# Kernel optimization log

Hardware: AMD Instinct MI355X
Metric: run time of the kernel (lower is better)

The kernel has to match this reference:

```python
import jax, jax.numpy as jnp
import numpy as np
from jax import lax

DIM = 8            # per-head dim
GROUPS = 192       # 3 * heads, groups of the pointwise aggreg conv
EPS_ATT = 1e-15
EPS_BN = 1e-5


def conv1x1(x, w):
    # x: (B,C,H,W), w: (O,C)
    return jnp.einsum('bchw,oc->bohw', x, w)


def setup_inputs() -> dict:
    key = jax.random.key(0)
    ks = jax.random.split(key, 9)
    B, C, H, W = 4, 512, 64, 64
    td3 = 3 * 512  # 3 * total_dim = 1536
    return {
        'x':       jax.random.normal(ks[0], (B, C, H, W), jnp.float32),
        'w_qkv':   jax.random.normal(ks[1], (td3, C), jnp.float32) * 0.05,
        'w_dw':    jax.random.normal(ks[2], (td3, 1, 5, 5), jnp.float32) * 0.05,
        'w_pw':    jax.random.normal(ks[3], (GROUPS, 8, 8), jnp.float32) * 0.05,
        'w_proj':  jax.random.normal(ks[4], (512, 1024), jnp.float32) * 0.05,
        'bn_gamma': 1.0 + 0.1 * jax.random.normal(ks[5], (512,), jnp.float32),
        'bn_beta': 0.1 * jax.random.normal(ks[6], (512,), jnp.float32),
        'bn_mean': 0.1 * jax.random.normal(ks[7], (512,), jnp.float32),
        'bn_var':  0.5 + jax.random.uniform(ks[8], (512,), jnp.float32),
    }


def reference(x, w_qkv, w_dw, w_pw, w_proj, bn_gamma, bn_beta, bn_mean, bn_var):
    B, _, H, W = x.shape
    # qkv 1x1 conv (no norm / act)
    qkv = conv1x1(x, w_qkv)                      # (B,1536,H,W)
    # multi-scale aggreg branch: depthwise 5x5 then grouped 1x1
    y = lax.conv_general_dilated(
        qkv, w_dw, window_strides=(1, 1), padding=((2, 2), (2, 2)),
        feature_group_count=qkv.shape[1],
        dimension_numbers=('NCHW', 'OIHW', 'NCHW'))
    yg = y.reshape(B, GROUPS, 8, H, W)
    y = jnp.einsum('bgihw,goi->bgohw', yg, w_pw).reshape(B, -1, H, W)
    ms = jnp.concatenate([qkv, y], axis=1)       # (B,3072,H,W)

    # relu linear attention (fp32)
    N = H * W
    t = ms.astype(jnp.float32).reshape(B, -1, 3 * DIM, N)   # (B,128,24,N)
    q = jax.nn.relu(t[:, :, :DIM])               # (B,h,8,N)
    k = jax.nn.relu(t[:, :, DIM:2 * DIM])        # (B,h,8,N)
    v = t[:, :, 2 * DIM:]                        # (B,h,8,N)
    v = jnp.concatenate([v, jnp.ones_like(v[:, :, :1])], axis=2)  # (B,h,9,N)
    vk = jnp.einsum('bhdn,bhen->bhde', v, k)     # (B,h,9,8)
    out = jnp.einsum('bhde,bhen->bhdn', vk, q)   # (B,h,9,N)
    out = out[:, :, :DIM] / (out[:, :, DIM:] + EPS_ATT)
    out = out.reshape(B, -1, H, W).astype(ms.dtype)  # (B,1024,H,W)

    # proj 1x1 conv + BatchNorm2d (inference, running stats)
    p = conv1x1(out, w_proj)                     # (B,512,H,W)
    scale = (bn_gamma / jnp.sqrt(bn_var + EPS_BN))[None, :, None, None]
    shift = (bn_beta - bn_mean * bn_gamma / jnp.sqrt(bn_var + EPS_BN))[None, :, None, None]
    return p * scale + shift
```

## Files before the change

kernel.cpp:

```cpp
#include <hip/hip_runtime.h>
#include <cstddef>


#define NPIX 4096
#define TD3 1536

typedef _Float16 f16;
typedef __attribute__((ext_vector_type(8))) _Float16 v8h;
typedef __attribute__((ext_vector_type(4))) float v4f;
typedef unsigned short ushort_t;

#define GLL16(g, l) __builtin_amdgcn_global_load_lds(                         \
    (const __attribute__((address_space(1))) unsigned int*)(g),               \
    (__attribute__((address_space(3))) unsigned int*)(l), 16, 0, 0)

template <int SPLITB, int BN>
__global__ __launch_bounds__(256) void gemm_f16(
    const f16* __restrict__ Ah, const f16* __restrict__ Al,
    const f16* __restrict__ Bh, const f16* __restrict__ Bl,
    float* __restrict__ C, int M, int N, int K,
    const float* __restrict__ bn_g, const float* __restrict__ bn_b,
    const float* __restrict__ bn_m, const float* __restrict__ bn_v)
{
    __shared__ f16 AsH[128 * 32];
    __shared__ f16 AsL[128 * 32];
    __shared__ f16 BsH[128 * 32];
    __shared__ f16 BsL[SPLITB ? 128 * 32 : 64];

    const int tid  = threadIdx.x;
    const int lane = tid & 63;
    const int w    = tid >> 6;
    const int wm   = w >> 1, wn = w & 1;
    const int mBase = blockIdx.y * 128, nBase = blockIdx.x * 128;
    Bh += (size_t)blockIdx.z * N * K;
    if (SPLITB) Bl += (size_t)blockIdx.z * N * K;
    C  += (size_t)blockIdx.z * M * N;

    const f16* gAh[2]; const f16* gAl[2]; const f16* gBh[2]; const f16* gBl[2];
    int ldsOff[2];
    #pragma unroll
    for (int p = 0; p < 2; ++p) {
        int off = (w * 2 + p) * 1024 + lane * 16;
        int r  = off >> 6;
        int ci = (off & 63) >> 1;
        gAh[p] = Ah + (size_t)(mBase + r) * K + ci;
        gAl[p] = Al + (size_t)(mBase + r) * K + ci;
        gBh[p] = Bh + (size_t)(nBase + r) * K + ci;
        if (SPLITB) gBl[p] = Bl + (size_t)(nBase + r) * K + ci;
        ldsOff[p] = (w * 2 + p) * 512;
    }

    v4f acc[4][4];
    #pragma unroll
    for (int i = 0; i < 4; ++i)
        #pragma unroll
        for (int j = 0; j < 4; ++j)
            acc[i][j] = (v4f){0.f, 0.f, 0.f, 0.f};

    const int kq = lane >> 4;
    const int rm = lane & 15;
    const int KT = K >> 5;
    for (int kt = 0; kt < KT; ++kt) {
        #pragma unroll
        for (int p = 0; p < 2; ++p) {
            GLL16(gAh[p] + kt * 32, &AsH[ldsOff[p]]);
            GLL16(gAl[p] + kt * 32, &AsL[ldsOff[p]]);
            GLL16(gBh[p] + kt * 32, &BsH[ldsOff[p]]);
            if (SPLITB) GLL16(gBl[p] + kt * 32, &BsL[ldsOff[p]]);
        }
        __syncthreads();

        v8h ah[4], al[4], bh[4], bl[4];
        #pragma unroll
        for (int i = 0; i < 4; ++i) {
            ah[i] = *(const v8h*)&AsH[(wm * 64 + i * 16 + rm) * 32 + kq * 8];
            al[i] = *(const v8h*)&AsL[(wm * 64 + i * 16 + rm) * 32 + kq * 8];
            bh[i] = *(const v8h*)&BsH[(wn * 64 + i * 16 + rm) * 32 + kq * 8];
            if (SPLITB)
                bl[i] = *(const v8h*)&BsL[(wn * 64 + i * 16 + rm) * 32 + kq * 8];
        }
        #pragma unroll
        for (int i = 0; i < 4; ++i)
            #pragma unroll
            for (int j = 0; j < 4; ++j) {
                acc[i][j] = __builtin_amdgcn_mfma_f32_16x16x32_f16(
                    ah[i], bh[j], acc[i][j], 0, 0, 0);
                acc[i][j] = __builtin_amdgcn_mfma_f32_16x16x32_f16(
                    al[i], bh[j], acc[i][j], 0, 0, 0);
                if (SPLITB)
                    acc[i][j] = __builtin_amdgcn_mfma_f32_16x16x32_f16(
                        ah[i], bl[j], acc[i][j], 0, 0, 0);
            }
        __syncthreads();
    }

    const int rq = lane >> 4, cn = lane & 15;
    #pragma unroll
    for (int i = 0; i < 4; ++i) {
        #pragma unroll
        for (int rg = 0; rg < 4; ++rg) {
            int row = mBase + wm * 64 + i * 16 + rq * 4 + rg;
            float sc = 1.f, sh = 0.f;
            if (BN) {
                sc = bn_g[row] * rsqrtf(bn_v[row] + 1e-5f);
                sh = bn_b[row] - bn_m[row] * sc;
            }
            #pragma unroll
            for (int j = 0; j < 4; ++j) {
                int col = nBase + wn * 64 + j * 16 + cn;
                float v = acc[i][j][rg];
                C[(size_t)row * N + col] = BN ? (v * sc + sh) : v;
            }
        }
    }
}

__global__ __launch_bounds__(256) void cvt_split(
    const float* __restrict__ src, f16* __restrict__ dh, f16* __restrict__ dl,
    int n4)
{
    int i = blockIdx.x * 256 + threadIdx.x;
    if (i < n4) {
        float4 f = ((const float4*)src)[i];
        f16 h[4], l[4];
        float ff[4] = {f.x, f.y, f.z, f.w};
        #pragma unroll
        for (int q = 0; q < 4; ++q) {
            h[q] = (f16)ff[q];
            l[q] = (f16)(ff[q] - (float)h[q]);
        }
        *(uint2*)&dh[(size_t)i * 4] = *(uint2*)h;
        *(uint2*)&dl[(size_t)i * 4] = *(uint2*)l;
    }
}

__global__ __launch_bounds__(256) void transp_split(
    const float* __restrict__ src, f16* __restrict__ dh, f16* __restrict__ dl)
{
    __shared__ float t[64][65];
    const int tid = threadIdx.x;
    const int n0 = blockIdx.x * 64, c0 = blockIdx.y * 64, b = blockIdx.z;

    const int row = tid >> 2;
    const int nn  = (tid & 3) * 16;
    const float* sp = src + ((size_t)b * 512 + c0 + row) * NPIX + n0 + nn;
    #pragma unroll
    for (int q = 0; q < 4; ++q) {
        float4 f = *(const float4*)(sp + q * 4);
        t[row][nn + q * 4 + 0] = f.x;
        t[row][nn + q * 4 + 1] = f.y;
        t[row][nn + q * 4 + 2] = f.z;
        t[row][nn + q * 4 + 3] = f.w;
    }
    __syncthreads();

    const int nrow = tid >> 2;
    const int cc   = (tid & 3) * 16;
    f16 h[16], l[16];
    #pragma unroll
    for (int q = 0; q < 16; ++q) {
        float f = t[cc + q][nrow];
        h[q] = (f16)f;
        l[q] = (f16)(f - (float)h[q]);
    }
    size_t di = ((size_t)b * NPIX + n0 + nrow) * 512 + c0 + cc;
    *(uint4*)&dh[di] = *(uint4*)&h[0];
    *(uint4*)&dh[di + 8] = *(uint4*)&h[8];
    *(uint4*)&dl[di] = *(uint4*)&l[0];
    *(uint4*)&dl[di + 8] = *(uint4*)&l[8];
}

__global__ __launch_bounds__(256) void dwpw(
    const float* __restrict__ qkv, const float* __restrict__ w_dw,
    const float* __restrict__ w_pw, float* __restrict__ y)
{
    __shared__ float tile[8][36][68];

    const int tid = threadIdx.x;
    const int g = blockIdx.y;
    const int b = blockIdx.z;
    const int h0 = blockIdx.x * 32;
    const size_t cbase = (size_t)b * TD3 + g * 8;

    for (int idx = tid; idx < 288; idx += 256) {
        int ch = idx / 36, r = idx - ch * 36;
        *(float2*)&tile[ch][r][0]  = (float2){0.f, 0.f};
        *(float2*)&tile[ch][r][66] = (float2){0.f, 0.f};
    }
    #pragma unroll
    for (int it = 0; it < 18; ++it) {
        int idx = tid + it * 256;
        int ch = idx / 576;
        int rem = idx - ch * 576;
        int r = rem >> 4, q = rem & 15;
        int gh = h0 + r - 2;
        float4 v = {0.f, 0.f, 0.f, 0.f};
        if (gh >= 0 && gh < 64)
            v = *(const float4*)&qkv[(cbase + ch) * NPIX + gh * 64 + q * 4];
        *(float2*)&tile[ch][r][2 + q * 4] = (float2){v.x, v.y};
        *(float2*)&tile[ch][r][4 + q * 4] = (float2){v.z, v.w};
    }
    __syncthreads();

    const int wc0 = (tid & 15) * 4;
    const int rp  = tid >> 4;

    float acc[8][8];
    #pragma unroll
    for (int o = 0; o < 8; ++o)
        #pragma unroll
        for (int p = 0; p < 8; ++p) acc[o][p] = 0.f;

    #pragma unroll
    for (int ch = 0; ch < 8; ++ch) {
        const float* wdg = w_dw + (size_t)(g * 8 + ch) * 25;
        float wdr[25];
        #pragma unroll
        for (int t = 0; t < 25; ++t) wdr[t] = wdg[t];
        float wpr[8];
        #pragma unroll
        for (int o = 0; o < 8; ++o) wpr[o] = w_pw[g * 64 + o * 8 + ch];

        float w[6][8];
        #pragma unroll
        for (int rr = 0; rr < 6; ++rr) {
            *(float4*)&w[rr][0] = *(const float4*)&tile[ch][rp * 2 + rr][wc0];
            *(float4*)&w[rr][4] = *(const float4*)&tile[ch][rp * 2 + rr][wc0 + 4];
        }

        float dwv[8];
        #pragma unroll
        for (int s = 0; s < 2; ++s)
            #pragma unroll
            for (int cc = 0; cc < 4; ++cc) {
                float sum = 0.f;
                #pragma unroll
                for (int di = 0; di < 5; ++di)
                    #pragma unroll
                    for (int dj = 0; dj < 5; ++dj)
                        sum = fmaf(w[s + di][cc + dj], wdr[di * 5 + dj], sum);
                dwv[s * 4 + cc] = sum;
            }
        #pragma unroll
        for (int o = 0; o < 8; ++o)
            #pragma unroll
            for (int p = 0; p < 8; ++p)
                acc[o][p] = fmaf(dwv[p], wpr[o], acc[o][p]);
    }

    #pragma unroll
    for (int o = 0; o < 8; ++o)
        #pragma unroll
        for (int s = 0; s < 2; ++s) {
            float4 v = {acc[o][s * 4 + 0], acc[o][s * 4 + 1],
                        acc[o][s * 4 + 2], acc[o][s * 4 + 3]};
            *(float4*)&y[(cbase + o) * NPIX + (h0 + rp * 2 + s) * 64 + wc0] = v;
        }
}

__global__ __launch_bounds__(256) void attn_stats(
    const float* __restrict__ qkv, const float* __restrict__ yy,
    float* __restrict__ vkout)
{
    const int h = blockIdx.x;
    const int b = blockIdx.y;
    const float* src = (h < 64)
        ? qkv + ((size_t)b * TD3 + h * 24) * NPIX
        : yy  + ((size_t)b * TD3 + (h - 64) * 24) * NPIX;

    float acc[9][8];
    #pragma unroll
    for (int d = 0; d < 9; ++d)
        #pragma unroll
        for (int e = 0; e < 8; ++e) acc[d][e] = 0.f;

    for (int n = threadIdx.x; n < NPIX; n += 256) {
        float kr[8], vv[8];
        #pragma unroll
        for (int e = 0; e < 8; ++e) kr[e] = fmaxf(src[(8 + e) * NPIX + n], 0.f);
        #pragma unroll
        for (int d = 0; d < 8; ++d) vv[d] = src[(16 + d) * NPIX + n];
        #pragma unroll
        for (int d = 0; d < 8; ++d)
            #pragma unroll
            for (int e = 0; e < 8; ++e) acc[d][e] = fmaf(vv[d], kr[e], acc[d][e]);
        #pragma unroll
        for (int e = 0; e < 8; ++e) acc[8][e] += kr[e];
    }

    __shared__ float part[4][72];
    const int lane = threadIdx.x & 63, wave = threadIdx.x >> 6;
    #pragma unroll
    for (int i = 0; i < 72; ++i) {
        float v = acc[i / 8][i % 8];
        #pragma unroll
        for (int off = 32; off; off >>= 1) v += __shfl_down(v, off, 64);
        if (lane == 0) part[wave][i] = v;
    }
    __syncthreads();
    if (threadIdx.x < 72) {
        float v = part[0][threadIdx.x] + part[1][threadIdx.x] +
                  part[2][threadIdx.x] + part[3][threadIdx.x];
        vkout[((size_t)b * 128 + h) * 72 + threadIdx.x] = v;
    }
}

__global__ __launch_bounds__(256) void attn_apply_t(
    const float* __restrict__ qkv, const float* __restrict__ yy,
    const float* __restrict__ vkin, f16* __restrict__ attout)
{
    const int h = blockIdx.y;
    const int b = blockIdx.z;
    const int n = blockIdx.x * 256 + threadIdx.x;

    __shared__ float vk[72];
    if (threadIdx.x < 72)
        vk[threadIdx.x] = vkin[((size_t)b * 128 + h) * 72 + threadIdx.x];
    __syncthreads();

    const float* src = (h < 64)
        ? qkv + ((size_t)b * TD3 + h * 24) * NPIX
        : yy  + ((size_t)b * TD3 + (h - 64) * 24) * NPIX;

    float qr[8];
    #pragma unroll
    for (int e = 0; e < 8; ++e) qr[e] = fmaxf(src[e * NPIX + n], 0.f);

    float den = 0.f;
    #pragma unroll
    for (int e = 0; e < 8; ++e) den = fmaf(vk[64 + e], qr[e], den);
    float inv = 1.f / (den + 1e-15f);

    f16 o[8];
    #pragma unroll
    for (int d = 0; d < 8; ++d) {
        float num = 0.f;
        #pragma unroll
        for (int e = 0; e < 8; ++e) num = fmaf(vk[d * 8 + e], qr[e], num);
        o[d] = (f16)(num * inv);
    }
    *(uint4*)&attout[((size_t)b * NPIX + n) * 1024 + h * 8] = *(uint4*)o;
}

extern "C" void kernel_launch(void* const* d_in, const int* in_sizes, int n_in,
                              void* d_out, int out_size, void* d_ws, size_t ws_size,
                              hipStream_t stream)
{
    (void)in_sizes; (void)n_in; (void)out_size; (void)ws_size;
    const float* x      = (const float*)d_in[0];
    const float* w_qkv  = (const float*)d_in[1];
    const float* w_dw   = (const float*)d_in[2];
    const float* w_pw   = (const float*)d_in[3];
    const float* w_proj = (const float*)d_in[4];
    const float* bn_g   = (const float*)d_in[5];
    const float* bn_b   = (const float*)d_in[6];
    const float* bn_m   = (const float*)d_in[7];
    const float* bn_v   = (const float*)d_in[8];
    float* out = (float*)d_out;

    char* ws = (char*)d_ws;
    float* qkv     = (float*)(ws);
    float* y       = (float*)(ws + 100663296);
    f16*   x_t_h   = (f16*)(ws + 201326592);
    f16*   x_t_l   = (f16*)(ws + 218103808);
    f16*   attout  = (f16*)(ws + 201326592);
    f16*   w_qkv_h = (f16*)(ws + 234881024);
    f16*   w_qkv_l = (f16*)(ws + 236453888);
    f16*   w_proj_h= (f16*)(ws + 238026752);
    f16*   w_proj_l= (f16*)(ws + 239075328);
    float* vk      = out;

    cvt_split<<<768, 256, 0, stream>>>(w_qkv, w_qkv_h, w_qkv_l, 196608);
    cvt_split<<<512, 256, 0, stream>>>(w_proj, w_proj_h, w_proj_l, 131072);
    transp_split<<<dim3(64, 8, 4), 256, 0, stream>>>(x, x_t_h, x_t_l);
    gemm_f16<1, 0><<<dim3(32, 12, 4), 256, 0, stream>>>(
        w_qkv_h, w_qkv_l, x_t_h, x_t_l, qkv, 1536, 4096, 512,
        nullptr, nullptr, nullptr, nullptr);
    dwpw<<<dim3(2, 192, 4), 256, 0, stream>>>(qkv, w_dw, w_pw, y);
    attn_stats<<<dim3(128, 4), 256, 0, stream>>>(qkv, y, vk);
    attn_apply_t<<<dim3(16, 128, 4), 256, 0, stream>>>(qkv, y, vk, attout);
    gemm_f16<0, 1><<<dim3(32, 4, 4), 256, 0, stream>>>(
        w_proj_h, w_proj_l, attout, nullptr, out, 512, 4096, 1024,
        bn_g, bn_b, bn_m, bn_v);
}
```

Before: 336.7 us.

## Double-buffer B tiles in LDS with XOR swizzle; load A fragments directly from global

The GEMM now keeps only the B operand in LDS, double-buffered so the next k-tile is prefetched while the current one is computed, with an XOR swizzle on the LDS layout to avoid bank conflicts. The A hi/lo fragments are read straight from global memory into registers instead of being staged through LDS. Launch bounds now request 3 blocks per CU. The aim is to cut LDS traffic and footprint and to hide load latency, at the cost of uncoalesced global reads for A and heavier register pressure.

```diff
diff --git a/kernel.cpp b/kernel.cpp
--- a/kernel.cpp
+++ b/kernel.cpp
@@ -15,17 +15,15 @@
     (__attribute__((address_space(3))) unsigned int*)(l), 16, 0, 0)
 
 template <int SPLITB, int BN>
-__global__ __launch_bounds__(256) void gemm_f16(
+__global__ __launch_bounds__(256, 3) void gemm_f16(
     const f16* __restrict__ Ah, const f16* __restrict__ Al,
     const f16* __restrict__ Bh, const f16* __restrict__ Bl,
     float* __restrict__ C, int M, int N, int K,
     const float* __restrict__ bn_g, const float* __restrict__ bn_b,
     const float* __restrict__ bn_m, const float* __restrict__ bn_v)
 {
-    __shared__ f16 AsH[128 * 32];
-    __shared__ f16 AsL[128 * 32];
-    __shared__ f16 BsH[128 * 32];
-    __shared__ f16 BsL[SPLITB ? 128 * 32 : 64];
+    __shared__ f16 BsH[2][128 * 32];
+    __shared__ f16 BsL[SPLITB ? 2 : 1][SPLITB ? 128 * 32 : 64];
 
     const int tid  = threadIdx.x;
     const int lane = tid & 63;
@@ -36,20 +34,28 @@
     if (SPLITB) Bl += (size_t)blockIdx.z * N * K;
     C  += (size_t)blockIdx.z * M * N;
 
-    const f16* gAh[2]; const f16* gAl[2]; const f16* gBh[2]; const f16* gBl[2];
+    const f16* gBh[2]; const f16* gBl[2];
     int ldsOff[2];
     #pragma unroll
     for (int p = 0; p < 2; ++p) {
-        int off = (w * 2 + p) * 1024 + lane * 16;
-        int r  = off >> 6;
-        int ci = (off & 63) >> 1;
-        gAh[p] = Ah + (size_t)(mBase + r) * K + ci;
-        gAl[p] = Al + (size_t)(mBase + r) * K + ci;
+        int phys = (w * 2 + p) * 1024 + lane * 16;
+        int lgc  = phys ^ (((phys >> 7) & 3) << 4);
+        int r  = lgc >> 6;
+        int ci = (lgc & 63) >> 1;
         gBh[p] = Bh + (size_t)(nBase + r) * K + ci;
         if (SPLITB) gBl[p] = Bl + (size_t)(nBase + r) * K + ci;
         ldsOff[p] = (w * 2 + p) * 512;
     }
 
+    const int kq = lane >> 4;
+    const int rm = lane & 15;
+    const int slot = kq ^ ((rm >> 1) & 3);
+
+    size_t aoff[4];
+    #pragma unroll
+    for (int i = 0; i < 4; ++i)
+        aoff[i] = (size_t)(mBase + wm * 64 + i * 16 + rm) * K + kq * 8;
+
     v4f acc[4][4];
     #pragma unroll
     for (int i = 0; i < 4; ++i)
@@ -57,27 +63,37 @@
         for (int j = 0; j < 4; ++j)
             acc[i][j] = (v4f){0.f, 0.f, 0.f, 0.f};
 
-    const int kq = lane >> 4;
-    const int rm = lane & 15;
     const int KT = K >> 5;
+
+    #pragma unroll
+    for (int p = 0; p < 2; ++p) {
+        GLL16(gBh[p], &BsH[0][ldsOff[p]]);
+        if (SPLITB) GLL16(gBl[p], &BsL[0][ldsOff[p]]);
+    }
+    __syncthreads();
+
     for (int kt = 0; kt < KT; ++kt) {
-        #pragma unroll
-        for (int p = 0; p < 2; ++p) {
-            GLL16(gAh[p] + kt * 32, &AsH[ldsOff[p]]);
-            GLL16(gAl[p] + kt * 32, &AsL[ldsOff[p]]);
-            GLL16(gBh[p] + kt * 32, &BsH[ldsOff[p]]);
-            if (SPLITB) GLL16(gBl[p] + kt * 32, &BsL[ldsOff[p]]);
-        }
-        __syncthreads();
+        const int cb = kt & 1, nb = cb ^ 1;
+        if (kt + 1 < KT) {
+            #pragma unroll
+            for (int p = 0; p < 2; ++p) {
+                GLL16(gBh[p] + (kt + 1) * 32, &BsH[nb][ldsOff[p]]);
+                if (SPLITB) GLL16(gBl[p] + (kt + 1) * 32, &BsL[nb][ldsOff[p]]);
+            }
+        }
 
         v8h ah[4], al[4], bh[4], bl[4];
         #pragma unroll
         for (int i = 0; i < 4; ++i) {
-            ah[i] = *(const v8h*)&AsH[(wm * 64 + i * 16 + rm) * 32 + kq * 8];
-            al[i] = *(const v8h*)&AsL[(wm * 64 + i * 16 + rm) * 32 + kq * 8];
-            bh[i] = *(const v8h*)&BsH[(wn * 64 + i * 16 + rm) * 32 + kq * 8];
+            ah[i] = *(const v8h*)(Ah + aoff[i] + kt * 32);
+            al[i] = *(const v8h*)(Al + aoff[i] + kt * 32);
+        }
+        #pragma unroll
+        for (int j = 0; j < 4; ++j) {
+            int row = wn * 64 + j * 16 + rm;
+            bh[j] = *(const v8h*)&BsH[cb][row * 32 + slot * 8];
             if (SPLITB)
-                bl[i] = *(const v8h*)&BsL[(wn * 64 + i * 16 + rm) * 32 + kq * 8];
+                bl[j] = *(const v8h*)&BsL[cb][row * 32 + slot * 8];
         }
         #pragma unroll
         for (int i = 0; i < 4; ++i)
```

Result: slower. 410.8 us (+22.0%).
